# Performance work log

Measured on AMD Instinct MI355X. Metric: run time of the kernel, lower is better.

Reference implementation:

```python
import jax, jax.numpy as jnp
import numpy as np

DIAG = 4  # number of distinct power-of-2 diagonal bands; must divide H


def _diag_mask(H, L):
    # head h in group g = h // (H // DIAG) uses tril diagonal offset 2**g - 1.
    # True entries are MASKED (filled with -inf), except the last key column
    # which is always kept (cur_mask[:, -1] = 0 in the torch code).
    group = H // DIAG
    offs = 2 ** (jnp.arange(H) // group) - 1            # [H]
    rows = jnp.arange(L)[:, None]                        # [L,1] query index
    cols = jnp.arange(L)[None, :]                        # [1,L] key index
    mask = (cols <= rows + offs[:, None, None]) & (cols != L - 1)  # [H,L,L]
    return mask


def setup_inputs() -> dict:
    key = jax.random.key(0)
    kq, kk, kv = jax.random.split(key, 3)
    B, L, H, E = 4, 2048, 16, 64
    queries = jax.random.normal(kq, (B, L, H, E), dtype=jnp.float32)
    keys = jax.random.normal(kk, (B, L, H, E), dtype=jnp.float32)
    values = jax.random.normal(kv, (B, L, H, E), dtype=jnp.float32)
    return {"queries": queries, "keys": keys, "values": values}


def reference(queries, keys, values):
    B, L, H, E = queries.shape
    scale = 1.0 / np.sqrt(E).astype(np.float32)
    # [B,H,L,S]
    scores = jnp.einsum('blhe,bshe->bhls', queries, keys)
    mask = _diag_mask(H, L)                              # [H,L,L]
    scores = jnp.where(mask[None], -jnp.inf, scores)
    A = jax.nn.softmax(scale * scores, axis=-1)          # dropout inactive (eval)
    V = jnp.einsum('bhls,bshd->blhd', A, values)
    return V
```

## Files before the change

kernel.cpp:

```cpp
#include <hip/hip_runtime.h>
#include <stdint.h>

using f32x4  = __attribute__((ext_vector_type(4))) float;
using f32x16 = __attribute__((ext_vector_type(16))) float;
using s16x8  = __attribute__((ext_vector_type(8))) short;
using u16x4  = __attribute__((ext_vector_type(4))) unsigned short;
using u32x4  = __attribute__((ext_vector_type(4))) unsigned int;

typedef __attribute__((address_space(3))) unsigned int lds_u32;
typedef __attribute__((address_space(1))) unsigned int glb_u32;

__device__ __forceinline__ unsigned short f2bf(float f){
  union { float f; unsigned u; } x; x.f = f;
  return (unsigned short)((x.u + 0x7FFFu + ((x.u >> 16) & 1u)) >> 16);
}
__device__ __forceinline__ unsigned cvt_pk(float lo, float hi){
  unsigned r;
  asm("v_cvt_pk_bf16_f32 %0, %1, %2" : "=v"(r) : "v"(lo), "v"(hi));
  return r;
}
__device__ __forceinline__ void plswap(unsigned &a, unsigned &b){
  asm volatile("v_permlane32_swap_b32 %0, %1" : "+v"(a), "+v"(b));
}

#if __has_builtin(__builtin_amdgcn_exp2f)
#define EXP2F(x) __builtin_amdgcn_exp2f(x)
#else
#define EXP2F(x) exp2f(x)
#endif

#define MFMA16(A,B,C) __builtin_amdgcn_mfma_f32_16x16x32_bf16((A),(B),(C),0,0,0)
#define MFMA32(A,B,C) __builtin_amdgcn_mfma_f32_32x32x16_bf16((A),(B),(C),0,0,0)

constexpr int   L      = 2048;
constexpr int   H      = 16;
constexpr int   E      = 64;
constexpr int   HE     = 1024;
constexpr float SCALE  = 0.125f;
constexpr float QSCALE = 0.18033688011112042f;

__global__ __launch_bounds__(256)
void prep_kv(const float* __restrict__ Kg, const float* __restrict__ Vg,
             unsigned short* __restrict__ Ko, unsigned short* __restrict__ Vo){
  __shared__ __align__(16) unsigned short t8[4096];
  const int g0 = blockIdx.x;
  const int t  = threadIdx.x;
  if (g0 < 2048){
    const int gid = g0;
    const int jt = gid & 31, bh = gid >> 5;
    const int b = bh >> 4, h = bh & 15;
    const int key6 = t >> 2;
    const int p    = t & 3;
    const int kb = key6 >> 5, k31 = key6 & 31;
    const float* src = Kg + ((size_t)((b*2048 + jt*64 + key6)*16 + h) << 6) + p*16;
    const float4 v0 = *reinterpret_cast<const float4*>(src);
    const float4 v1 = *reinterpret_cast<const float4*>(src + 4);
    const float4 v2 = *reinterpret_cast<const float4*>(src + 8);
    const float4 v3 = *reinterpret_cast<const float4*>(src + 12);
    s16x8 f0, f1;
    f0[0]=(short)f2bf(v0.x); f0[1]=(short)f2bf(v0.y); f0[2]=(short)f2bf(v0.z); f0[3]=(short)f2bf(v0.w);
    f0[4]=(short)f2bf(v1.x); f0[5]=(short)f2bf(v1.y); f0[6]=(short)f2bf(v1.z); f0[7]=(short)f2bf(v1.w);
    f1[0]=(short)f2bf(v2.x); f1[1]=(short)f2bf(v2.y); f1[2]=(short)f2bf(v2.z); f1[3]=(short)f2bf(v2.w);
    f1[4]=(short)f2bf(v3.x); f1[5]=(short)f2bf(v3.y); f1[6]=(short)f2bf(v3.z); f1[7]=(short)f2bf(v3.w);
    const int slot0 = ((kb*4 + p)*2 + 0)*32 + k31;
    *reinterpret_cast<s16x8*>(&t8[slot0*8])      = f0;
    *reinterpret_cast<s16x8*>(&t8[(slot0+32)*8]) = f1;
    __syncthreads();
    unsigned short* dst = Ko + ((size_t)gid << 12) + t*16;
    *reinterpret_cast<s16x8*>(dst)     = *reinterpret_cast<const s16x8*>(&t8[t*16]);
    *reinterpret_cast<s16x8*>(dst + 8) = *reinterpret_cast<const s16x8*>(&t8[t*16 + 8]);
  } else {
    const int gid = g0 - 2048;
    const int jt = gid & 31, bh = gid >> 5;
    const int b = bh >> 4, h = bh & 15;
    const int key6 = t >> 2;
    const int p    = t & 3;
    const int kc = key6 >> 4, h2 = (key6 >> 3) & 1, kr = key6 & 7;
    const float* src = Vg + ((size_t)((b*2048 + jt*64 + key6)*16 + h) << 6) + p*16;
    float vv[16];
    #pragma unroll
    for (int q = 0; q < 4; ++q){
      const float4 v = *reinterpret_cast<const float4*>(src + q*4);
      vv[q*4+0]=v.x; vv[q*4+1]=v.y; vv[q*4+2]=v.z; vv[q*4+3]=v.w;
    }
    #pragma unroll
    for (int j = 0; j < 16; ++j){
      const int e  = p*16 + j;
      const int eb = e >> 5, e31 = e & 31;
      const int slot = ((eb*4 + kc)*2 + h2)*32 + e31;
      t8[slot*8 + kr] = f2bf(vv[j]);
    }
    __syncthreads();
    unsigned short* dst = Vo + ((size_t)gid << 12) + t*16;
    *reinterpret_cast<s16x8*>(dst)     = *reinterpret_cast<const s16x8*>(&t8[t*16]);
    *reinterpret_cast<s16x8*>(dst + 8) = *reinterpret_cast<const s16x8*>(&t8[t*16 + 8]);
  }
}

__global__ __launch_bounds__(256, 4)
void attn6(const float* __restrict__ Qg, const unsigned short* __restrict__ Kbg,
           const unsigned short* __restrict__ Vtg, float* __restrict__ Og)
{
  __shared__ __align__(16) unsigned short Kbuf[2][4096];
  __shared__ __align__(16) unsigned short Vbuf[2][4096];

  const int tid  = threadIdx.x;
  const int wave = tid >> 6;
  const int lane = tid & 63;
  const int c    = lane & 31;
  const int hi   = lane >> 5;

  const int gid = blockIdx.x;
  const int qb  = gid >> 6;
  const int bh  = gid & 63;
  const int b = bh >> 4, h = bh & 15;
  const int off = (1 << (h >> 2)) - 1;

  const int    r0    = 128 * qb;
  const int    qrow0 = r0 + wave * 32;
  const size_t fbase = (size_t)b * L * HE + (size_t)h * 64;
  const size_t tbase = (size_t)bh * 32;

  s16x8 qf[4];
  {
    const float* qp_ = Qg + fbase + (size_t)(qrow0 + c) * HE;
    #pragma unroll
    for (int ec = 0; ec < 4; ++ec){
      const float4 a  = *reinterpret_cast<const float4*>(qp_ + ec*16 + hi*8);
      const float4 b2 = *reinterpret_cast<const float4*>(qp_ + ec*16 + hi*8 + 4);
      s16x8 v;
      v[0]=(short)f2bf(a.x*QSCALE);  v[1]=(short)f2bf(a.y*QSCALE);
      v[2]=(short)f2bf(a.z*QSCALE);  v[3]=(short)f2bf(a.w*QSCALE);
      v[4]=(short)f2bf(b2.x*QSCALE); v[5]=(short)f2bf(b2.y*QSCALE);
      v[6]=(short)f2bf(b2.z*QSCALE); v[7]=(short)f2bf(b2.w*QSCALE);
      qf[ec] = v;
    }
  }

  s16x8 ones;
  #pragma unroll
  for (int j = 0; j < 8; ++j) ones[j] = (short)0x3F80;

  f32x16 acc0, acc1, accl;
  #pragma unroll
  for (int r = 0; r < 16; ++r){ acc0[r]=0.f; acc1[r]=0.f; accl[r]=0.f; }

  const int j0   = 2 * qb;
  const int qlim = qrow0 + c + off;

  auto STAGE = [&](int jt, int nb){
    const unsigned short* gk = Kbg + ((size_t)(tbase + jt) << 12) + (size_t)(wave*128 + lane)*8;
    const unsigned short* gv = Vtg + ((size_t)(tbase + jt) << 12) + (size_t)(wave*128 + lane)*8;
    __builtin_amdgcn_global_load_lds((const glb_u32*)gk,        (lds_u32*)&Kbuf[nb][wave*1024],       16, 0, 0);
    __builtin_amdgcn_global_load_lds((const glb_u32*)(gk+512),  (lds_u32*)&Kbuf[nb][wave*1024 + 512], 16, 0, 0);
    __builtin_amdgcn_global_load_lds((const glb_u32*)gv,        (lds_u32*)&Vbuf[nb][wave*1024],       16, 0, 0);
    __builtin_amdgcn_global_load_lds((const glb_u32*)(gv+512),  (lds_u32*)&Vbuf[nb][wave*1024 + 512], 16, 0, 0);
  };

  auto COMP = [&](int jt, int nb){
    const int s0 = jt * 64;
    if ((jt < 31) && (s0 + 63 <= qrow0 + off)) return;
    const unsigned short* KB = Kbuf[nb];
    const unsigned short* VB = Vbuf[nb];

    f32x16 S0, S1;
    #pragma unroll
    for (int r = 0; r < 16; ++r){ S0[r]=0.f; S1[r]=0.f; }
    __builtin_amdgcn_s_setprio(1);
    #pragma unroll
    for (int ec = 0; ec < 4; ++ec){
      const s16x8 k0 = *reinterpret_cast<const s16x8*>(&KB[(((0*4+ec)*2+hi)*32 + c)*8]);
      const s16x8 k1 = *reinterpret_cast<const s16x8*>(&KB[(((1*4+ec)*2+hi)*32 + c)*8]);
      S0 = MFMA32(k0, qf[ec], S0);
      S1 = MFMA32(k1, qf[ec], S1);
    }
    __builtin_amdgcn_s_setprio(0);

    if ((jt == 31) || (s0 <= qrow0 + 31 + off)){
      #pragma unroll
      for (int r = 0; r < 16; ++r){
        const int kg0 = s0 + (r&3) + 8*(r>>2) + 4*hi;
        const int kg1 = kg0 + 32;
        if (!((kg0 > qlim) || (kg0 == L-1))) S0[r] = -1e30f;
        if (!((kg1 > qlim) || (kg1 == L-1))) S1[r] = -1e30f;
      }
    }

    #pragma unroll
    for (int r = 0; r < 16; ++r){
      S0[r] = EXP2F(S0[r]);
      S1[r] = EXP2F(S1[r]);
    }

    __builtin_amdgcn_s_setprio(1);
    #define PV_STEP(Pv, kh, kcg) { \
      unsigned a0 = cvt_pk(Pv[8*(kh)+0], Pv[8*(kh)+1]); \
      unsigned a1 = cvt_pk(Pv[8*(kh)+2], Pv[8*(kh)+3]); \
      unsigned b0 = cvt_pk(Pv[8*(kh)+4], Pv[8*(kh)+5]); \
      unsigned b1 = cvt_pk(Pv[8*(kh)+6], Pv[8*(kh)+7]); \
      plswap(a0, b0); plswap(a1, b1); \
      u32x4 afu; afu[0]=a0; afu[1]=a1; afu[2]=b0; afu[3]=b1; \
      const s16x8 af = __builtin_bit_cast(s16x8, afu); \
      const s16x8 vf0 = *reinterpret_cast<const s16x8*>(&VB[(((0*4+(kcg))*2+hi)*32 + c)*8]); \
      const s16x8 vf1 = *reinterpret_cast<const s16x8*>(&VB[(((1*4+(kcg))*2+hi)*32 + c)*8]); \
      acc0 = MFMA32(af, vf0, acc0); \
      acc1 = MFMA32(af, vf1, acc1); \
      accl = MFMA32(af, ones, accl); \
    }
    PV_STEP(S0, 0, 0)
    PV_STEP(S0, 1, 1)
    PV_STEP(S1, 0, 2)
    PV_STEP(S1, 1, 3)
    #undef PV_STEP
    __builtin_amdgcn_s_setprio(0);
  };

  #define WAITBAR4 asm volatile("s_waitcnt vmcnt(4)\n\ts_barrier" ::: "memory")
  #define WAITBAR0 asm volatile("s_waitcnt vmcnt(0)\n\ts_barrier" ::: "memory")
  #define BARRIER  asm volatile("s_barrier" ::: "memory")

  STAGE(j0, 0);
  STAGE(j0 + 1, 1);

  for (int jt = j0; jt < 30; jt += 2){
    WAITBAR4;
    COMP(jt, 0);
    BARRIER;
    STAGE(jt + 2, 0);
    WAITBAR4;
    COMP(jt + 1, 1);
    BARRIER;
    STAGE(jt + 3, 1);
  }
  WAITBAR4;
  COMP(30, 0);
  WAITBAR0;
  COMP(31, 1);

  #undef WAITBAR4
  #undef WAITBAR0
  #undef BARRIER

  #pragma unroll
  for (int r = 0; r < 16; ++r){
    const int rowr = (r&3) + 8*(r>>2) + 4*hi;
    const float li = 1.0f / accl[r];
    float* op = Og + fbase + (size_t)(qrow0 + rowr) * HE;
    op[c]      = acc0[r] * li;
    op[32 + c] = acc1[r] * li;
  }
}

__global__ __launch_bounds__(512)
void attn_band(const float* __restrict__ Qg, const float* __restrict__ Kg,
               const float* __restrict__ Vg, float* __restrict__ Og)
{
  __shared__ __align__(16) unsigned short Ks[64*64];
  __shared__ __align__(16) unsigned short Vs[64*64];
  __shared__ __align__(16) unsigned short Ps[8][16*64];
  const int tid  = threadIdx.x;
  const int wave = tid >> 6;
  const int lane = tid & 63;
  const int lo16 = lane & 15;
  const int hi4  = lane >> 4;
  const int gid = blockIdx.x;
  const int qb  = gid & 15;
  const int bh  = gid >> 4;
  const int b   = bh >> 4;
  const int h   = bh & 15;
  const int off = (1 << (h >> 2)) - 1;
  const int    r0   = qb * 128;
  const size_t base = (size_t)b * L * HE + (size_t)h * 64;
  const int qrow0 = r0 + wave * 16;
  s16x8 qf[2];
  {
    const float* qp = Qg + base + (size_t)(qrow0 + lo16) * HE;
    #pragma unroll
    for (int ec = 0; ec < 2; ++ec){
      const int e0 = ec*32 + hi4*8;
      s16x8 v;
      #pragma unroll
      for (int j = 0; j < 8; ++j) v[j] = (short)f2bf(qp[e0 + j]);
      qf[ec] = v;
    }
  }
  f32x4 acc[4];
  #pragma unroll
  for (int et = 0; et < 4; ++et) acc[et] = f32x4{0.f,0.f,0.f,0.f};
  float m_run[4], l_run[4];
  #pragma unroll
  for (int i = 0; i < 4; ++i){ m_run[i] = -1e30f; l_run[i] = 0.f; }
  const int j0 = (r0 + off + 1) >> 6;
  for (int jt = j0; jt < 32; ++jt){
    const int s0 = jt * 64;
    __syncthreads();
    {
      const int f4    = tid & 15;
      const int rbase = tid >> 4;
      #pragma unroll
      for (int p = 0; p < 2; ++p){
        const int row = p*32 + rbase;
        const float4 vv = *reinterpret_cast<const float4*>(
            Kg + base + (size_t)(s0 + row) * HE + f4*4);
        u16x4 w; w[0]=f2bf(vv.x); w[1]=f2bf(vv.y); w[2]=f2bf(vv.z); w[3]=f2bf(vv.w);
        const int idx = row*64 + ((f4*4) ^ ((row & 7) << 3));
        *reinterpret_cast<u16x4*>(&Ks[idx]) = w;
      }
    }
    {
      const int kb = tid >> 5;
      const int e0 = (tid & 31) * 2;
      float2 cc[4];
      #pragma unroll
      for (int j = 0; j < 4; ++j)
        cc[j] = *reinterpret_cast<const float2*>(
            Vg + base + (size_t)(s0 + 4*kb + j) * HE + e0);
      #pragma unroll
      for (int i = 0; i < 2; ++i){
        const int e = e0 + i;
        u16x4 w;
        w[0] = f2bf(i ? cc[0].y : cc[0].x);
        w[1] = f2bf(i ? cc[1].y : cc[1].x);
        w[2] = f2bf(i ? cc[2].y : cc[2].x);
        w[3] = f2bf(i ? cc[3].y : cc[3].x);
        const int idx = e*64 + ((kb*4) ^ ((e & 7) << 3));
        *reinterpret_cast<u16x4*>(&Vs[idx]) = w;
      }
    }
    __syncthreads();
    if (jt < 31 && s0 + 63 <= qrow0 + off) continue;
    f32x4 S[4];
    #pragma unroll
    for (int kt = 0; kt < 4; ++kt){
      const int key = kt*16 + lo16;
      f32x4 z = {0.f,0.f,0.f,0.f};
      #pragma unroll
      for (int ec = 0; ec < 2; ++ec){
        const int e = ec*32 + hi4*8;
        const s16x8 kf = *reinterpret_cast<const s16x8*>(
            &Ks[key*64 + (e ^ ((key & 7) << 3))]);
        z = MFMA16(qf[ec], kf, z);
      }
      S[kt] = z;
    }
    #pragma unroll
    for (int kt = 0; kt < 4; ++kt){
      const int kg = s0 + kt*16 + lo16;
      #pragma unroll
      for (int i = 0; i < 4; ++i){
        const int qg2 = qrow0 + hi4*4 + i;
        const bool ok = (kg > qg2 + off) || (kg == L-1);
        S[kt][i] = ok ? S[kt][i]*SCALE : -1e30f;
      }
    }
    #pragma unroll
    for (int i = 0; i < 4; ++i){
      float t = fmaxf(fmaxf(S[0][i],S[1][i]), fmaxf(S[2][i],S[3][i]));
      t = fmaxf(t, __shfl_xor(t,1));
      t = fmaxf(t, __shfl_xor(t,2));
      t = fmaxf(t, __shfl_xor(t,4));
      t = fmaxf(t, __shfl_xor(t,8));
      const float mn = fmaxf(m_run[i], t);
      const float rs = __expf(m_run[i] - mn);
      m_run[i]  = mn;
      l_run[i] *= rs;
      acc[0][i] *= rs; acc[1][i] *= rs; acc[2][i] *= rs; acc[3][i] *= rs;
    }
    unsigned short* pwv = Ps[wave];
    float rsum[4] = {0.f,0.f,0.f,0.f};
    #pragma unroll
    for (int kt = 0; kt < 4; ++kt){
      #pragma unroll
      for (int i = 0; i < 4; ++i){
        const float p = __expf(S[kt][i] - m_run[i]);
        rsum[i] += p;
        const int qr  = hi4*4 + i;
        const int col = kt*16 + lo16;
        pwv[qr*64 + (col ^ ((qr & 7) << 3))] = f2bf(p);
      }
    }
    #pragma unroll
    for (int i = 0; i < 4; ++i){
      float t = rsum[i];
      t += __shfl_xor(t,1); t += __shfl_xor(t,2);
      t += __shfl_xor(t,4); t += __shfl_xor(t,8);
      l_run[i] += t;
    }
    #pragma unroll
    for (int kc = 0; kc < 2; ++kc){
      const int kk = kc*32 + hi4*8;
      const s16x8 pf = *reinterpret_cast<const s16x8*>(
          &pwv[lo16*64 + (kk ^ ((lo16 & 7) << 3))]);
      #pragma unroll
      for (int et = 0; et < 4; ++et){
        const int e = et*16 + lo16;
        const s16x8 vf = *reinterpret_cast<const s16x8*>(
            &Vs[e*64 + (kk ^ ((e & 7) << 3))]);
        acc[et] = MFMA16(pf, vf, acc[et]);
      }
    }
  }
  #pragma unroll
  for (int i = 0; i < 4; ++i){
    const float inv = 1.0f / l_run[i];
    const int   qg2 = qrow0 + hi4*4 + i;
    float* op = Og + base + (size_t)qg2 * HE;
    #pragma unroll
    for (int et = 0; et < 4; ++et)
      op[et*16 + lo16] = acc[et][i] * inv;
  }
}

extern "C" void kernel_launch(void* const* d_in, const int* in_sizes, int n_in,
                              void* d_out, int out_size, void* d_ws, size_t ws_size,
                              hipStream_t stream) {
  const float* Q = (const float*)d_in[0];
  const float* K = (const float*)d_in[1];
  const float* V = (const float*)d_in[2];
  float* O = (float*)d_out;

  const size_t kb_bytes = (size_t)64 * 32 * 4096 * 2;
  const size_t need     = kb_bytes * 2;
  if (ws_size >= need) {
    unsigned short* Kb = (unsigned short*)d_ws;
    unsigned short* Vt = (unsigned short*)((char*)d_ws + kb_bytes);
    prep_kv<<<dim3(4096), dim3(256), 0, stream>>>(K, V, Kb, Vt);
    attn6  <<<dim3(1024), dim3(256), 0, stream>>>(Q, Kb, Vt, O);
  } else {
    attn_band<<<dim3(1024), dim3(512), 0, stream>>>(Q, K, V, O);
  }
}
```

Baseline: 72.58 us.

## Halve query rows per attention block and pipeline K/V stages one tile at a time

The attention kernel now uses 2-wave blocks covering 64 query rows, and the grid doubles to 2048 blocks. This gives finer work granularity and better load balance across the band-masked triangle. The double-buffered K/V staging loop now advances one tile per iteration, with each wave loading twice as much per stage. The per-wave tile skip is removed because 64-row blocks start at their diagonal tile. In exchange, each K/V tile is fetched from L2 by twice as many blocks.

After: 84.74 us. 16.8% more time.

```diff
diff --git a/kernel.cpp b/kernel.cpp
--- a/kernel.cpp
+++ b/kernel.cpp
@@ -97,9 +97,9 @@
   }
 }
 
-__global__ __launch_bounds__(256, 4)
-void attn6(const float* __restrict__ Qg, const unsigned short* __restrict__ Kbg,
-           const unsigned short* __restrict__ Vtg, float* __restrict__ Og)
+__global__ __launch_bounds__(128, 4)
+void attn12(const float* __restrict__ Qg, const unsigned short* __restrict__ Kbg,
+            const unsigned short* __restrict__ Vtg, float* __restrict__ Og)
 {
   __shared__ __align__(16) unsigned short Kbuf[2][4096];
   __shared__ __align__(16) unsigned short Vbuf[2][4096];
@@ -111,13 +111,12 @@
   const int hi   = lane >> 5;
 
   const int gid = blockIdx.x;
-  const int qb  = gid >> 6;
+  const int qc  = gid >> 6;
   const int bh  = gid & 63;
   const int b = bh >> 4, h = bh & 15;
   const int off = (1 << (h >> 2)) - 1;
 
-  const int    r0    = 128 * qb;
-  const int    qrow0 = r0 + wave * 32;
+  const int    qrow0 = 64 * qc + wave * 32;
   const size_t fbase = (size_t)b * L * HE + (size_t)h * 64;
   const size_t tbase = (size_t)bh * 32;
 
@@ -145,21 +144,24 @@
   #pragma unroll
   for (int r = 0; r < 16; ++r){ acc0[r]=0.f; acc1[r]=0.f; accl[r]=0.f; }
 
-  const int j0   = 2 * qb;
+  const int j0   = qc;
   const int qlim = qrow0 + c + off;
 
   auto STAGE = [&](int jt, int nb){
-    const unsigned short* gk = Kbg + ((size_t)(tbase + jt) << 12) + (size_t)(wave*128 + lane)*8;
-    const unsigned short* gv = Vtg + ((size_t)(tbase + jt) << 12) + (size_t)(wave*128 + lane)*8;
-    __builtin_amdgcn_global_load_lds((const glb_u32*)gk,        (lds_u32*)&Kbuf[nb][wave*1024],       16, 0, 0);
-    __builtin_amdgcn_global_load_lds((const glb_u32*)(gk+512),  (lds_u32*)&Kbuf[nb][wave*1024 + 512], 16, 0, 0);
-    __builtin_amdgcn_global_load_lds((const glb_u32*)gv,        (lds_u32*)&Vbuf[nb][wave*1024],       16, 0, 0);
-    __builtin_amdgcn_global_load_lds((const glb_u32*)(gv+512),  (lds_u32*)&Vbuf[nb][wave*1024 + 512], 16, 0, 0);
+    const unsigned short* gk = Kbg + ((size_t)(tbase + jt) << 12) + (size_t)(wave*2048 + lane*8);
+    const unsigned short* gv = Vtg + ((size_t)(tbase + jt) << 12) + (size_t)(wave*2048 + lane*8);
+    #pragma unroll
+    for (int i = 0; i < 4; ++i)
+      __builtin_amdgcn_global_load_lds((const glb_u32*)(gk + i*512),
+          (lds_u32*)&Kbuf[nb][wave*2048 + i*512], 16, 0, 0);
+    #pragma unroll
+    for (int i = 0; i < 4; ++i)
+      __builtin_amdgcn_global_load_lds((const glb_u32*)(gv + i*512),
+          (lds_u32*)&Vbuf[nb][wave*2048 + i*512], 16, 0, 0);
   };
 
   auto COMP = [&](int jt, int nb){
     const int s0 = jt * 64;
-    if ((jt < 31) && (s0 + 63 <= qrow0 + off)) return;
     const unsigned short* KB = Kbuf[nb];
     const unsigned short* VB = Vbuf[nb];
 
@@ -215,29 +217,28 @@
     __builtin_amdgcn_s_setprio(0);
   };
 
-  #define WAITBAR4 asm volatile("s_waitcnt vmcnt(4)\n\ts_barrier" ::: "memory")
+  #define WAITBAR8 asm volatile("s_waitcnt vmcnt(8)\n\ts_barrier" ::: "memory")
   #define WAITBAR0 asm volatile("s_waitcnt vmcnt(0)\n\ts_barrier" ::: "memory")
-  #define BARRIER  asm volatile("s_barrier" ::: "memory")
-
-  STAGE(j0, 0);
-  STAGE(j0 + 1, 1);
-
-  for (int jt = j0; jt < 30; jt += 2){
-    WAITBAR4;
-    COMP(jt, 0);
+  #define BARRIER  __builtin_amdgcn_s_barrier()
+
+  STAGE(j0, j0 & 1);
+  {
+    const int j1 = (j0 + 1 <= 31) ? (j0 + 1) : 31;
+    STAGE(j1, (j0 + 1) & 1);
+  }
+
+  for (int jt = j0; jt < 30; ++jt){
+    WAITBAR8;
+    COMP(jt, jt & 1);
     BARRIER;
-    STAGE(jt + 2, 0);
-    WAITBAR4;
-    COMP(jt + 1, 1);
-    BARRIER;
-    STAGE(jt + 3, 1);
-  }
-  WAITBAR4;
+    STAGE(jt + 2, jt & 1);
+  }
+  WAITBAR8;
   COMP(30, 0);
   WAITBAR0;
   COMP(31, 1);
 
-  #undef WAITBAR4
+  #undef WAITBAR8
   #undef WAITBAR0
   #undef BARRIER
 
@@ -425,7 +426,7 @@
     unsigned short* Kb = (unsigned short*)d_ws;
     unsigned short* Vt = (unsigned short*)((char*)d_ws + kb_bytes);
     prep_kv<<<dim3(4096), dim3(256), 0, stream>>>(K, V, Kb, Vt);
-    attn6  <<<dim3(1024), dim3(256), 0, stream>>>(Q, Kb, Vt, O);
+    attn12 <<<dim3(2048), dim3(128), 0, stream>>>(Q, Kb, Vt, O);
   } else {
     attn_band<<<dim3(1024), dim3(512), 0, stream>>>(Q, K, V, O);
   }
```
